# Kernel tuning notes

Hardware: AMD Instinct MI355X
Metric: run time of the kernel (lower is better)

Reference implementation:

```python
import jax, jax.numpy as jnp
import numpy as np

N = 50000   # nodes
E = 600000  # edges (before self loops)
D = 128     # in = hidden = out channels
EPS = 1e-5


def setup_inputs() -> dict:
    key = jax.random.key(0)
    ks = jax.random.split(key, 12)
    s = 1.0 / np.sqrt(D)
    inp = {
        "x": jax.random.normal(ks[0], (N, D), jnp.float32),
        "edge_index": jax.random.randint(ks[1], (2, E), 0, N, dtype=jnp.int64),
        "W1": jax.random.normal(ks[2], (D, D), jnp.float32) * s,
        "b1": jnp.zeros((D,), jnp.float32),
        "g1": jnp.ones((D,), jnp.float32),
        "be1": jnp.zeros((D,), jnp.float32),
        "W2": jax.random.normal(ks[3], (D, D), jnp.float32) * s,
        "b2": jnp.zeros((D,), jnp.float32),
        "g2": jnp.ones((D,), jnp.float32),
        "be2": jnp.zeros((D,), jnp.float32),
        "W3": jax.random.normal(ks[4], (D, D), jnp.float32) * s,
        "b3": jnp.zeros((D,), jnp.float32),
    }
    return inp


def _layer_norm(h, g, b):
    mu = jnp.mean(h, axis=-1, keepdims=True)
    var = jnp.mean(jnp.square(h - mu), axis=-1, keepdims=True)
    return (h - mu) * jax.lax.rsqrt(var + EPS) * g + b


def _gcn_layer(h, src, dst, ew, W, b, fill):
    # PyG gcn_norm: append internal self loops with weight `fill`
    loop = jnp.arange(N, dtype=src.dtype)
    s = jnp.concatenate([src, loop])
    d = jnp.concatenate([dst, loop])
    w = jnp.concatenate([ew, jnp.full((N,), fill, h.dtype)])
    deg = jax.ops.segment_sum(w, d, num_segments=N)
    dinv = jnp.where(deg > 0, jax.lax.rsqrt(deg), 0.0)
    norm = dinv[s] * w * dinv[d]  # [E_tot]
    hw = h @ W                    # [N, D]
    out = jax.ops.segment_sum(norm[:, None] * hw[s], d, num_segments=N)
    return out + b


def reference(x, edge_index, W1, b1, g1, be1, W2, b2, g2, be2, W3, b3):
    # outer add_self_loops with edge_weight = 1 (edge_attr is None path)
    loop = jnp.arange(N, dtype=edge_index.dtype)
    src = jnp.concatenate([edge_index[0], loop])
    dst = jnp.concatenate([edge_index[1], loop])
    ew = jnp.ones((E + N,), x.dtype)

    residual = x
    h = _gcn_layer(x, src, dst, ew, W1, b1, 2.0)   # improved=True
    h = jax.nn.relu(_layer_norm(h, g1, be1))
    h = _gcn_layer(h, src, dst, ew, W2, b2, 2.0)   # improved=True
    h = jax.nn.relu(_layer_norm(h, g2, be2))
    h = _gcn_layer(h, src, dst, ew, W3, b3, 1.0)   # improved=False
    return h + residual
```

## Files before the change

kernel.cpp:

```cpp
#include <hip/hip_runtime.h>
#include <hip/hip_bf16.h>
#include <cstdint>

#define N_NODES 50000
#define N_EDGES 600000
#define DCH     128
#define LN_EPS  1e-5f
#define CAP     64
#define CAPSH   6
#define SLICE_N (N_NODES + 1)

typedef __attribute__((ext_vector_type(8))) __bf16 bf16x8;
typedef __attribute__((ext_vector_type(4))) float  f32x4;
typedef __attribute__((ext_vector_type(4))) int          int4e;
typedef __attribute__((ext_vector_type(2))) unsigned int uint2e;

__device__ inline unsigned short f2bf(float f) {
    unsigned int b; __builtin_memcpy(&b, &f, 4);
    b = b + 0x7fffu + ((b >> 16) & 1u);
    return (unsigned short)(b >> 16);
}
__device__ inline float bf_lo(unsigned int u) {
    unsigned int t = u << 16; float f; __builtin_memcpy(&f, &t, 4); return f;
}
__device__ inline float bf_hi(unsigned int u) {
    unsigned int t = u & 0xffff0000u; float f; __builtin_memcpy(&f, &t, 4); return f;
}

__global__ __launch_bounds__(256) void fill_k(const int* __restrict__ ei,
                                              int* __restrict__ cnt, int* __restrict__ csr) {
    __shared__ int sbad;
    int tid = threadIdx.x;
    if (tid == 0) sbad = 0;
    __syncthreads();
    const long long* e64 = (const long long*)ei;
    long long v = e64[tid];
    long long w = e64[300000 + tid];
    if (v < 0 || v >= N_NODES || w < 0 || w >= N_NODES) sbad = 1;
    __syncthreads();
    int is64 = (sbad == 0);

    int e = blockIdx.x * 256 + tid;
    if (e >= N_EDGES) return;
    long long sv = is64 ? e64[e]           : (long long)ei[e];
    long long dv = is64 ? e64[N_EDGES + e] : (long long)ei[N_EDGES + e];
    int s = (int)(sv < 0 ? 0 : (sv >= N_NODES ? N_NODES - 1 : sv));
    int d = (int)(dv < 0 ? 0 : (dv >= N_NODES ? N_NODES - 1 : dv));
    int pos = atomicAdd(&cnt[d], 1);
    if (pos < CAP) csr[(d << CAPSH) + pos] = s;
}

#define CVT_T    ((N_NODES + 1) * 32)
#define DINV_OFF CVT_T
#define TRAN_OFF (DINV_OFF + N_NODES)
#define SENT_OFF (TRAN_OFF + 3 * 128 * 128)
#define PREP_T   (SENT_OFF + 128)

__global__ __launch_bounds__(256) void prep_k(
        const float* __restrict__ x, const int* __restrict__ cnt,
        const float* __restrict__ W1, const float* __restrict__ W2,
        const float* __restrict__ W3,
        unsigned short* __restrict__ xbf, float* __restrict__ dinv2,
        float* __restrict__ dinv1, unsigned short* __restrict__ Wt,
        unsigned short* __restrict__ hbuf) {
    int id = blockIdx.x * 256 + threadIdx.x;
    if (id < CVT_T) {
        int node = id >> 5;
        int co = (id & 31) * 4;
        int slice = co >> 5, off = co & 31;
        uint2 r; r.x = 0u; r.y = 0u;
        if (node < N_NODES) {
            float4 v = *(const float4*)(x + (size_t)node * DCH + co);
            float d = rsqrtf((float)cnt[node] + 3.0f);
            r.x = ((unsigned int)f2bf(v.y * d) << 16) | (unsigned int)f2bf(v.x * d);
            r.y = ((unsigned int)f2bf(v.w * d) << 16) | (unsigned int)f2bf(v.z * d);
        }
        *(uint2*)(xbf + ((size_t)slice * SLICE_N + node) * 32 + off) = r;
    } else if (id < TRAN_OFF) {
        int i = id - DINV_OFF;
        float c = (float)cnt[i];
        dinv2[i] = rsqrtf(c + 3.0f);
        dinv1[i] = rsqrtf(c + 2.0f);
    } else if (id < SENT_OFF) {
        int t = id - TRAN_OFF;
        int mat = t >> 14;
        int o = t & 16383;
        int n = o >> 7, k = o & 127;
        const float* W = (mat == 0) ? W1 : ((mat == 1) ? W2 : W3);
        Wt[t] = f2bf(W[k * 128 + n]);
    } else if (id < PREP_T) {
        int i = id - SENT_OFF;
        hbuf[((size_t)(i >> 5) * SLICE_N + N_NODES) * 32 + (i & 31)] = 0;
    }
}


__global__ __launch_bounds__(128) void agg_k(
        const unsigned short* __restrict__ hs, unsigned short* __restrict__ outb,
        const int* __restrict__ cnt, const int* __restrict__ csr,
        const float* __restrict__ dinv, float fillp1) {
    int slice = blockIdx.x & 3;
    int grp   = blockIdx.x >> 2;
    int wv    = threadIdx.x >> 6;
    int lane  = threadIdx.x & 63;
    int g     = lane >> 3;
    int l8    = lane & 7;
    int node  = grp * 16 + wv * 8 + g;

    const uint2* hp = (const uint2*)(hs + (size_t)slice * SLICE_N * 32);
    float di = dinv[node];
    int cn = cnt[node];
    int pc = (cn + 3) & ~3; if (pc > CAP) pc = CAP;
    pc = max(pc, __shfl_xor(pc, 8));
    pc = max(pc, __shfl_xor(pc, 16));
    pc = max(pc, __shfl_xor(pc, 32));

    const int4e* pcsr = (const int4e*)(csr + ((size_t)node << CAPSH));
    float a[4][4];
    #pragma unroll
    for (int j = 0; j < 4; j++)
        #pragma unroll
        for (int ch = 0; ch < 4; ch++) a[j][ch] = 0.f;

    for (int i = 0; i < pc; i += 4) {
        int4e e4 = __builtin_nontemporal_load(&pcsr[i >> 2]);
        int e0 = (i + 0 < cn) ? e4.x : N_NODES;
        int e1 = (i + 1 < cn) ? e4.y : N_NODES;
        int e2 = (i + 2 < cn) ? e4.z : N_NODES;
        int e3 = (i + 3 < cn) ? e4.w : N_NODES;
        uint2 u0 = hp[(size_t)e0 * 8 + l8];
        uint2 u1 = hp[(size_t)e1 * 8 + l8];
        uint2 u2 = hp[(size_t)e2 * 8 + l8];
        uint2 u3 = hp[(size_t)e3 * 8 + l8];
        a[0][0] += bf_lo(u0.x); a[0][1] += bf_hi(u0.x); a[0][2] += bf_lo(u0.y); a[0][3] += bf_hi(u0.y);
        a[1][0] += bf_lo(u1.x); a[1][1] += bf_hi(u1.x); a[1][2] += bf_lo(u1.y); a[1][3] += bf_hi(u1.y);
        a[2][0] += bf_lo(u2.x); a[2][1] += bf_hi(u2.x); a[2][2] += bf_lo(u2.y); a[2][3] += bf_hi(u2.y);
        a[3][0] += bf_lo(u3.x); a[3][1] += bf_hi(u3.x); a[3][2] += bf_lo(u3.y); a[3][3] += bf_hi(u3.y);
    }
    float c0 = (a[0][0] + a[1][0]) + (a[2][0] + a[3][0]);
    float c1 = (a[0][1] + a[1][1]) + (a[2][1] + a[3][1]);
    float c2 = (a[0][2] + a[1][2]) + (a[2][2] + a[3][2]);
    float c3 = (a[0][3] + a[1][3]) + (a[2][3] + a[3][3]);
    uint2 us = hp[(size_t)node * 8 + l8];
    c0 = di * (c0 + fillp1 * bf_lo(us.x));
    c1 = di * (c1 + fillp1 * bf_hi(us.x));
    c2 = di * (c2 + fillp1 * bf_lo(us.y));
    c3 = di * (c3 + fillp1 * bf_hi(us.y));
    uint2e res;
    res.x = ((unsigned int)f2bf(c1) << 16) | (unsigned int)f2bf(c0);
    res.y = ((unsigned int)f2bf(c3) << 16) | (unsigned int)f2bf(c2);
    __builtin_nontemporal_store(res,
        (uint2e*)(outb + (size_t)slice * SLICE_N * 32) + (size_t)node * 8 + l8);
}


template<int MODE>
__global__ __launch_bounds__(256) void gemm_k(
        const unsigned short* __restrict__ A,
        const unsigned short* __restrict__ Wt,
        const float* __restrict__ bias,
        const float* __restrict__ gamma,
        const float* __restrict__ beta,
        const float* __restrict__ dnext,
        const float* __restrict__ resid,
        unsigned short* __restrict__ out_bf,
        float* __restrict__ out_f) {
    int lane = threadIdx.x & 63;
    int wv   = threadIdx.x >> 6;
    int r0   = (blockIdx.x * 4 + wv) * 32;
    int m = lane & 15, q = lane >> 4;

    bf16x8 afr[2][4];
    #pragma unroll
    for (int mt = 0; mt < 2; mt++) {
        int arow = r0 + mt * 16 + m; if (arow >= N_NODES) arow = N_NODES - 1;
        #pragma unroll
        for (int kt = 0; kt < 4; kt++)
            afr[mt][kt] = __builtin_nontemporal_load(
                (const bf16x8*)(A + ((size_t)kt * SLICE_N + arow) * 32 + q * 8));
    }

    f32x4 acc[2][8];
    #pragma unroll
    for (int nt = 0; nt < 8; nt++) {
        f32x4 c0 = {0.f,0.f,0.f,0.f}, c1 = {0.f,0.f,0.f,0.f};
        const unsigned short* bp = Wt + (size_t)(nt * 16 + m) * DCH + q * 8;
        #pragma unroll
        for (int kt = 0; kt < 4; kt++) {
            bf16x8 bfr = *(const bf16x8*)(bp + kt * 32);
            c0 = __builtin_amdgcn_mfma_f32_16x16x32_bf16(afr[0][kt], bfr, c0, 0, 0, 0);
            c1 = __builtin_amdgcn_mfma_f32_16x16x32_bf16(afr[1][kt], bfr, c1, 0, 0, 0);
        }
        acc[0][nt] = c0; acc[1][nt] = c1;
    }

    float bv[8];
    #pragma unroll
    for (int nt = 0; nt < 8; nt++) bv[nt] = bias[nt * 16 + m];

    if (MODE == 0) {
        float gv[8], bev[8];
        #pragma unroll
        for (int nt = 0; nt < 8; nt++) { gv[nt] = gamma[nt*16+m]; bev[nt] = beta[nt*16+m]; }
        #pragma unroll
        for (int mt = 0; mt < 2; mt++) {
            #pragma unroll
            for (int nt = 0; nt < 8; nt++)
                #pragma unroll
                for (int r = 0; r < 4; r++) acc[mt][nt][r] += bv[nt];
            #pragma unroll
            for (int r = 0; r < 4; r++) {
                float s = 0.f, qs = 0.f;
                #pragma unroll
                for (int nt = 0; nt < 8; nt++) { float v = acc[mt][nt][r]; s += v; qs += v*v; }
                #pragma unroll
                for (int msk = 1; msk < 16; msk <<= 1) {
                    s  += __shfl_xor(s,  msk, 16);
                    qs += __shfl_xor(qs, msk, 16);
                }
                float mean = s * (1.f / 128.f);
                float var  = fmaxf(qs * (1.f / 128.f) - mean * mean, 0.f);
                float rstd = rsqrtf(var + LN_EPS);
                int row = r0 + mt * 16 + q * 4 + r;
                if (row < N_NODES) {
                    float dscale = dnext[row];
                    #pragma unroll
                    for (int nt = 0; nt < 8; nt++) {
                        float v = (acc[mt][nt][r] - mean) * rstd * gv[nt] + bev[nt];
                        v = fmaxf(v, 0.f) * dscale;
                        __builtin_nontemporal_store(f2bf(v),
                            out_bf + ((size_t)(nt >> 1) * SLICE_N + row) * 32
                                   + (nt & 1) * 16 + m);
                    }
                }
            }
        }
    } else {
        #pragma unroll
        for (int mt = 0; mt < 2; mt++)
            #pragma unroll
            for (int r = 0; r < 4; r++) {
                int row = r0 + mt * 16 + q * 4 + r;
                if (row < N_NODES) {
                    #pragma unroll
                    for (int nt = 0; nt < 8; nt++) {
                        float v = acc[mt][nt][r] + bv[nt]
                                + resid[(size_t)row * DCH + nt * 16 + m];
                        out_f[(size_t)row * DCH + nt * 16 + m] = v;
                    }
                }
            }
    }
}


extern "C" void kernel_launch(void* const* d_in, const int* in_sizes, int n_in,
                              void* d_out, int out_size, void* d_ws, size_t ws_size,
                              hipStream_t stream) {
    const float* x   = (const float*)d_in[0];
    const int*   ei  = (const int*)d_in[1];
    const float* W1  = (const float*)d_in[2];
    const float* b1  = (const float*)d_in[3];
    const float* g1  = (const float*)d_in[4];
    const float* be1 = (const float*)d_in[5];
    const float* W2  = (const float*)d_in[6];
    const float* b2  = (const float*)d_in[7];
    const float* g2  = (const float*)d_in[8];
    const float* be2 = (const float*)d_in[9];
    const float* W3  = (const float*)d_in[10];
    const float* b3  = (const float*)d_in[11];
    float* out = (float*)d_out;

    char* p = (char*)d_ws;
    auto alloc = [&](size_t bytes) -> void* {
        void* r = (void*)p; p += (bytes + 255) & ~(size_t)255; return r;
    };
    int*   cnt   = (int*)  alloc((size_t)N_NODES * 4);
    float* dinv2 = (float*)alloc((size_t)N_NODES * 4);
    float* dinv1 = (float*)alloc((size_t)N_NODES * 4);
    int*   csr   = (int*)  alloc((size_t)N_NODES * CAP * 4);
    unsigned short* Wt   = (unsigned short*)alloc((size_t)3 * 128 * 128 * 2);
    unsigned short* aggb = (unsigned short*)alloc((size_t)4 * SLICE_N * 32 * 2);
    unsigned short* xbf  = (unsigned short*)alloc((size_t)4 * SLICE_N * 32 * 2);
    unsigned short* hbuf = (unsigned short*)alloc((size_t)4 * SLICE_N * 32 * 2);

    (void)hipMemsetAsync(cnt, 0, (size_t)N_NODES * 4, stream);
    fill_k<<<(N_EDGES + 255) / 256, 256, 0, stream>>>(ei, cnt, csr);
    prep_k<<<(PREP_T + 255) / 256, 256, 0, stream>>>(x, cnt, W1, W2, W3,
                                                     xbf, dinv2, dinv1, Wt, hbuf);

    const int A_BLOCKS = 3125 * 4;
    const int G_BLOCKS = (N_NODES + 127) / 128;

    agg_k<<<A_BLOCKS, 128, 0, stream>>>(xbf, aggb, cnt, csr, dinv2, 3.0f);
    gemm_k<0><<<G_BLOCKS, 256, 0, stream>>>(aggb, Wt, b1, g1, be1, dinv2, nullptr, hbuf, nullptr);
    agg_k<<<A_BLOCKS, 128, 0, stream>>>(hbuf, aggb, cnt, csr, dinv2, 3.0f);
    gemm_k<0><<<G_BLOCKS, 256, 0, stream>>>(aggb, Wt + 16384, b2, g2, be2, dinv1, nullptr, hbuf, nullptr);
    agg_k<<<A_BLOCKS, 128, 0, stream>>>(hbuf, aggb, cnt, csr, dinv1, 2.0f);
    gemm_k<1><<<G_BLOCKS, 256, 0, stream>>>(aggb, Wt + 32768, b3, nullptr, nullptr, nullptr, x, nullptr, out);
}
```

Before: 298.0 us.

## Split CSR into four 16-slot buckets with uint16 indices, shrink GEMM row tile

```diff
diff --git a/kernel.cpp b/kernel.cpp
--- a/kernel.cpp
+++ b/kernel.cpp
@@ -8,11 +8,12 @@
 #define LN_EPS  1e-5f
 #define CAP     64
 #define CAPSH   6
+#define BCAP    16
 #define SLICE_N (N_NODES + 1)
 
 typedef __attribute__((ext_vector_type(8))) __bf16 bf16x8;
 typedef __attribute__((ext_vector_type(4))) float  f32x4;
-typedef __attribute__((ext_vector_type(4))) int          int4e;
+typedef __attribute__((ext_vector_type(8))) unsigned short u16x8;
 typedef __attribute__((ext_vector_type(2))) unsigned int uint2e;
 
 __device__ inline unsigned short f2bf(float f) {
@@ -28,7 +29,8 @@
 }
 
 __global__ __launch_bounds__(256) void fill_k(const int* __restrict__ ei,
-                                              int* __restrict__ cnt, int* __restrict__ csr) {
+                                              int* __restrict__ cnt4,
+                                              unsigned short* __restrict__ csr) {
     __shared__ int sbad;
     int tid = threadIdx.x;
     if (tid == 0) sbad = 0;
@@ -46,8 +48,9 @@
     long long dv = is64 ? e64[N_EDGES + e] : (long long)ei[N_EDGES + e];
     int s = (int)(sv < 0 ? 0 : (sv >= N_NODES ? N_NODES - 1 : sv));
     int d = (int)(dv < 0 ? 0 : (dv >= N_NODES ? N_NODES - 1 : dv));
-    int pos = atomicAdd(&cnt[d], 1);
-    if (pos < CAP) csr[(d << CAPSH) + pos] = s;
+    int b = e & 3;
+    int pos = atomicAdd(&cnt4[b * N_NODES + d], 1);
+    if (pos < BCAP) csr[(d << CAPSH) + (b << 4) + pos] = (unsigned short)s;
 }
 
 #define CVT_T    ((N_NODES + 1) * 32)
@@ -57,7 +60,7 @@
 #define PREP_T   (SENT_OFF + 128)
 
 __global__ __launch_bounds__(256) void prep_k(
-        const float* __restrict__ x, const int* __restrict__ cnt,
+        const float* __restrict__ x, const int* __restrict__ cnt4,
         const float* __restrict__ W1, const float* __restrict__ W2,
         const float* __restrict__ W3,
         unsigned short* __restrict__ xbf, float* __restrict__ dinv2,
@@ -71,16 +74,19 @@
         uint2 r; r.x = 0u; r.y = 0u;
         if (node < N_NODES) {
             float4 v = *(const float4*)(x + (size_t)node * DCH + co);
-            float d = rsqrtf((float)cnt[node] + 3.0f);
+            int c = cnt4[node] + cnt4[N_NODES + node]
+                  + cnt4[2 * N_NODES + node] + cnt4[3 * N_NODES + node];
+            float d = rsqrtf((float)c + 3.0f);
             r.x = ((unsigned int)f2bf(v.y * d) << 16) | (unsigned int)f2bf(v.x * d);
             r.y = ((unsigned int)f2bf(v.w * d) << 16) | (unsigned int)f2bf(v.z * d);
         }
         *(uint2*)(xbf + ((size_t)slice * SLICE_N + node) * 32 + off) = r;
     } else if (id < TRAN_OFF) {
         int i = id - DINV_OFF;
-        float c = (float)cnt[i];
-        dinv2[i] = rsqrtf(c + 3.0f);
-        dinv1[i] = rsqrtf(c + 2.0f);
+        int c = cnt4[i] + cnt4[N_NODES + i]
+              + cnt4[2 * N_NODES + i] + cnt4[3 * N_NODES + i];
+        dinv2[i] = rsqrtf((float)c + 3.0f);
+        dinv1[i] = rsqrtf((float)c + 2.0f);
     } else if (id < SENT_OFF) {
         int t = id - TRAN_OFF;
         int mat = t >> 14;
@@ -94,10 +100,9 @@
     }
 }
 
-
 __global__ __launch_bounds__(128) void agg_k(
         const unsigned short* __restrict__ hs, unsigned short* __restrict__ outb,
-        const int* __restrict__ cnt, const int* __restrict__ csr,
+        const int* __restrict__ cnt4, const unsigned short* __restrict__ csr,
         const float* __restrict__ dinv, float fillp1) {
     int slice = blockIdx.x & 3;
     int grp   = blockIdx.x >> 2;
@@ -109,46 +114,74 @@
 
     const uint2* hp = (const uint2*)(hs + (size_t)slice * SLICE_N * 32);
     float di = dinv[node];
-    int cn = cnt[node];
-    int pc = (cn + 3) & ~3; if (pc > CAP) pc = CAP;
-    pc = max(pc, __shfl_xor(pc, 8));
-    pc = max(pc, __shfl_xor(pc, 16));
-    pc = max(pc, __shfl_xor(pc, 32));
-
-    const int4e* pcsr = (const int4e*)(csr + ((size_t)node << CAPSH));
+    int bc0 = min(cnt4[node], BCAP);
+    int bc1 = min(cnt4[N_NODES + node], BCAP);
+    int bc2 = min(cnt4[2 * N_NODES + node], BCAP);
+    int bc3 = min(cnt4[3 * N_NODES + node], BCAP);
+
+    const u16x8* pcsr = (const u16x8*)(csr + ((size_t)node << CAPSH));
+    u16x8 c0 = __builtin_nontemporal_load(pcsr + 0);
+    u16x8 c1 = __builtin_nontemporal_load(pcsr + 2);
+    u16x8 c2 = __builtin_nontemporal_load(pcsr + 4);
+    u16x8 c3 = __builtin_nontemporal_load(pcsr + 6);
+
     float a[4][4];
     #pragma unroll
-    for (int j = 0; j < 4; j++)
-        #pragma unroll
-        for (int ch = 0; ch < 4; ch++) a[j][ch] = 0.f;
-
-    for (int i = 0; i < pc; i += 4) {
-        int4e e4 = __builtin_nontemporal_load(&pcsr[i >> 2]);
-        int e0 = (i + 0 < cn) ? e4.x : N_NODES;
-        int e1 = (i + 1 < cn) ? e4.y : N_NODES;
-        int e2 = (i + 2 < cn) ? e4.z : N_NODES;
-        int e3 = (i + 3 < cn) ? e4.w : N_NODES;
-        uint2 u0 = hp[(size_t)e0 * 8 + l8];
-        uint2 u1 = hp[(size_t)e1 * 8 + l8];
-        uint2 u2 = hp[(size_t)e2 * 8 + l8];
-        uint2 u3 = hp[(size_t)e3 * 8 + l8];
-        a[0][0] += bf_lo(u0.x); a[0][1] += bf_hi(u0.x); a[0][2] += bf_lo(u0.y); a[0][3] += bf_hi(u0.y);
-        a[1][0] += bf_lo(u1.x); a[1][1] += bf_hi(u1.x); a[1][2] += bf_lo(u1.y); a[1][3] += bf_hi(u1.y);
-        a[2][0] += bf_lo(u2.x); a[2][1] += bf_hi(u2.x); a[2][2] += bf_lo(u2.y); a[2][3] += bf_hi(u2.y);
-        a[3][0] += bf_lo(u3.x); a[3][1] += bf_hi(u3.x); a[3][2] += bf_lo(u3.y); a[3][3] += bf_hi(u3.y);
-    }
-    float c0 = (a[0][0] + a[1][0]) + (a[2][0] + a[3][0]);
-    float c1 = (a[0][1] + a[1][1]) + (a[2][1] + a[3][1]);
-    float c2 = (a[0][2] + a[1][2]) + (a[2][2] + a[3][2]);
-    float c3 = (a[0][3] + a[1][3]) + (a[2][3] + a[3][3]);
+    for (int k = 0; k < 4; k++)
+        #pragma unroll
+        for (int ch = 0; ch < 4; ch++) a[k][ch] = 0.f;
+
+    int eidx[32];
+    #pragma unroll
+    for (int j = 0; j < 8; j++) {
+        eidx[j]      = (j < bc0) ? (int)c0[j] : N_NODES;
+        eidx[8 + j]  = (j < bc1) ? (int)c1[j] : N_NODES;
+        eidx[16 + j] = (j < bc2) ? (int)c2[j] : N_NODES;
+        eidx[24 + j] = (j < bc3) ? (int)c3[j] : N_NODES;
+    }
+    #pragma unroll
+    for (int t = 0; t < 32; t++) {
+        uint2 u = hp[(size_t)eidx[t] * 8 + l8];
+        int k = t & 3;
+        a[k][0] += bf_lo(u.x); a[k][1] += bf_hi(u.x);
+        a[k][2] += bf_lo(u.y); a[k][3] += bf_hi(u.y);
+    }
+
+    int bm = max(max(bc0, bc1), max(bc2, bc3));
+    if (__any(bm > 8)) {
+        u16x8 d0 = __builtin_nontemporal_load(pcsr + 1);
+        u16x8 d1 = __builtin_nontemporal_load(pcsr + 3);
+        u16x8 d2 = __builtin_nontemporal_load(pcsr + 5);
+        u16x8 d3 = __builtin_nontemporal_load(pcsr + 7);
+        int fidx[32];
+        #pragma unroll
+        for (int j = 0; j < 8; j++) {
+            fidx[j]      = (8 + j < bc0) ? (int)d0[j] : N_NODES;
+            fidx[8 + j]  = (8 + j < bc1) ? (int)d1[j] : N_NODES;
+            fidx[16 + j] = (8 + j < bc2) ? (int)d2[j] : N_NODES;
+            fidx[24 + j] = (8 + j < bc3) ? (int)d3[j] : N_NODES;
+        }
+        #pragma unroll
+        for (int t = 0; t < 32; t++) {
+            uint2 u = hp[(size_t)fidx[t] * 8 + l8];
+            int k = t & 3;
+            a[k][0] += bf_lo(u.x); a[k][1] += bf_hi(u.x);
+            a[k][2] += bf_lo(u.y); a[k][3] += bf_hi(u.y);
+        }
+    }
+
+    float s0 = (a[0][0] + a[1][0]) + (a[2][0] + a[3][0]);
+    float s1 = (a[0][1] + a[1][1]) + (a[2][1] + a[3][1]);
+    float s2 = (a[0][2] + a[1][2]) + (a[2][2] + a[3][2]);
+    float s3 = (a[0][3] + a[1][3]) + (a[2][3] + a[3][3]);
     uint2 us = hp[(size_t)node * 8 + l8];
-    c0 = di * (c0 + fillp1 * bf_lo(us.x));
-    c1 = di * (c1 + fillp1 * bf_hi(us.x));
-    c2 = di * (c2 + fillp1 * bf_lo(us.y));
-    c3 = di * (c3 + fillp1 * bf_hi(us.y));
+    s0 = di * (s0 + fillp1 * bf_lo(us.x));
+    s1 = di * (s1 + fillp1 * bf_hi(us.x));
+    s2 = di * (s2 + fillp1 * bf_lo(us.y));
+    s3 = di * (s3 + fillp1 * bf_hi(us.y));
     uint2e res;
-    res.x = ((unsigned int)f2bf(c1) << 16) | (unsigned int)f2bf(c0);
-    res.y = ((unsigned int)f2bf(c3) << 16) | (unsigned int)f2bf(c2);
+    res.x = ((unsigned int)f2bf(s1) << 16) | (unsigned int)f2bf(s0);
+    res.y = ((unsigned int)f2bf(s3) << 16) | (unsigned int)f2bf(s2);
     __builtin_nontemporal_store(res,
         (uint2e*)(outb + (size_t)slice * SLICE_N * 32) + (size_t)node * 8 + l8);
 }
@@ -167,31 +200,27 @@
         float* __restrict__ out_f) {
     int lane = threadIdx.x & 63;
     int wv   = threadIdx.x >> 6;
-    int r0   = (blockIdx.x * 4 + wv) * 32;
+    int r0   = (blockIdx.x * 4 + wv) * 16;
     int m = lane & 15, q = lane >> 4;
 
-    bf16x8 afr[2][4];
-    #pragma unroll
-    for (int mt = 0; mt < 2; mt++) {
-        int arow = r0 + mt * 16 + m; if (arow >= N_NODES) arow = N_NODES - 1;
-        #pragma unroll
-        for (int kt = 0; kt < 4; kt++)
-            afr[mt][kt] = __builtin_nontemporal_load(
-                (const bf16x8*)(A + ((size_t)kt * SLICE_N + arow) * 32 + q * 8));
-    }
-
-    f32x4 acc[2][8];
+    bf16x8 afr[4];
+    int arow = r0 + m; if (arow >= N_NODES) arow = N_NODES - 1;
+    #pragma unroll
+    for (int kt = 0; kt < 4; kt++)
+        afr[kt] = __builtin_nontemporal_load(
+            (const bf16x8*)(A + ((size_t)kt * SLICE_N + arow) * 32 + q * 8));
+
+    f32x4 acc[8];
     #pragma unroll
     for (int nt = 0; nt < 8; nt++) {
-        f32x4 c0 = {0.f,0.f,0.f,0.f}, c1 = {0.f,0.f,0.f,0.f};
+        f32x4 c0 = {0.f, 0.f, 0.f, 0.f};
         const unsigned short* bp = Wt + (size_t)(nt * 16 + m) * DCH + q * 8;
         #pragma unroll
         for (int kt = 0; kt < 4; kt++) {
             bf16x8 bfr = *(const bf16x8*)(bp + kt * 32);
-            c0 = __builtin_amdgcn_mfma_f32_16x16x32_bf16(afr[0][kt], bfr, c0, 0, 0, 0);
-            c1 = __builtin_amdgcn_mfma_f32_16x16x32_bf16(afr[1][kt], bfr, c1, 0, 0, 0);
-        }
-        acc[0][nt] = c0; acc[1][nt] = c1;
+            c0 = __builtin_amdgcn_mfma_f32_16x16x32_bf16(afr[kt], bfr, c0, 0, 0, 0);
+        }
+        acc[nt] = c0;
     }
 
     float bv[8];
@@ -203,53 +232,48 @@
         #pragma unroll
         for (int nt = 0; nt < 8; nt++) { gv[nt] = gamma[nt*16+m]; bev[nt] = beta[nt*16+m]; }
         #pragma unroll
-        for (int mt = 0; mt < 2; mt++) {
+        for (int nt = 0; nt < 8; nt++)
             #pragma unroll
-            for (int nt = 0; nt < 8; nt++)
+            for (int r = 0; r < 4; r++) acc[nt][r] += bv[nt];
+        #pragma unroll
+        for (int r = 0; r < 4; r++) {
+            float s = 0.f, qs = 0.f;
+            #pragma unroll
+            for (int nt = 0; nt < 8; nt++) { float v = acc[nt][r]; s += v; qs += v*v; }
+            #pragma unroll
+            for (int msk = 1; msk < 16; msk <<= 1) {
+                s  += __shfl_xor(s,  msk, 16);
+                qs += __shfl_xor(qs, msk, 16);
+            }
+            float mean = s * (1.f / 128.f);
+            float var  = fmaxf(qs * (1.f / 128.f) - mean * mean, 0.f);
+            float rstd = rsqrtf(var + LN_EPS);
+            int row = r0 + q * 4 + r;
+            if (row < N_NODES) {
+                float dscale = dnext[row];
                 #pragma unroll
-                for (int r = 0; r < 4; r++) acc[mt][nt][r] += bv[nt];
-            #pragma unroll
-            for (int r = 0; r < 4; r++) {
-                float s = 0.f, qs = 0.f;
-                #pragma unroll
-                for (int nt = 0; nt < 8; nt++) { float v = acc[mt][nt][r]; s += v; qs += v*v; }
-                #pragma unroll
-                for (int msk = 1; msk < 16; msk <<= 1) {
-                    s  += __shfl_xor(s,  msk, 16);
-                    qs += __shfl_xor(qs, msk, 16);
-                }
-                float mean = s * (1.f / 128.f);
-                float var  = fmaxf(qs * (1.f / 128.f) - mean * mean, 0.f);
-                float rstd = rsqrtf(var + LN_EPS);
-                int row = r0 + mt * 16 + q * 4 + r;
-                if (row < N_NODES) {
-                    float dscale = dnext[row];
-                    #pragma unroll
-                    for (int nt = 0; nt < 8; nt++) {
-                        float v = (acc[mt][nt][r] - mean) * rstd * gv[nt] + bev[nt];
-                        v = fmaxf(v, 0.f) * dscale;
-                        __builtin_nontemporal_store(f2bf(v),
-                            out_bf + ((size_t)(nt >> 1) * SLICE_N + row) * 32
-                                   + (nt & 1) * 16 + m);
-                    }
+                for (int nt = 0; nt < 8; nt++) {
+                    float v = (acc[nt][r] - mean) * rstd * gv[nt] + bev[nt];
+                    v = fmaxf(v, 0.f) * dscale;
+                    __builtin_nontemporal_store(f2bf(v),
+                        out_bf + ((size_t)(nt >> 1) * SLICE_N + row) * 32
+                               + (nt & 1) * 16 + m);
                 }
             }
         }
     } else {
         #pragma unroll
-        for (int mt = 0; mt < 2; mt++)
-            #pragma unroll
-            for (int r = 0; r < 4; r++) {
-                int row = r0 + mt * 16 + q * 4 + r;
-                if (row < N_NODES) {
-                    #pragma unroll
-                    for (int nt = 0; nt < 8; nt++) {
-                        float v = acc[mt][nt][r] + bv[nt]
-                                + resid[(size_t)row * DCH + nt * 16 + m];
-                        out_f[(size_t)row * DCH + nt * 16 + m] = v;
-                    }
+        for (int r = 0; r < 4; r++) {
+            int row = r0 + q * 4 + r;
+            if (row < N_NODES) {
+                #pragma unroll
+                for (int nt = 0; nt < 8; nt++) {
+                    float v = acc[nt][r] + bv[nt]
+                            + resid[(size_t)row * DCH + nt * 16 + m];
+                    out_f[(size_t)row * DCH + nt * 16 + m] = v;
                 }
             }
+        }
     }
 }
 
@@ -275,27 +299,27 @@
     auto alloc = [&](size_t bytes) -> void* {
         void* r = (void*)p; p += (bytes + 255) & ~(size_t)255; return r;
     };
-    int*   cnt   = (int*)  alloc((size_t)N_NODES * 4);
+    int*   cnt4  = (int*)  alloc((size_t)4 * N_NODES * 4);
     float* dinv2 = (float*)alloc((size_t)N_NODES * 4);
     float* dinv1 = (float*)alloc((size_t)N_NODES * 4);
-    int*   csr   = (int*)  alloc((size_t)N_NODES * CAP * 4);
+    unsigned short* csr = (unsigned short*)alloc((size_t)N_NODES * CAP * 2);
     unsigned short* Wt   = (unsigned short*)alloc((size_t)3 * 128 * 128 * 2);
     unsigned short* aggb = (unsigned short*)alloc((size_t)4 * SLICE_N * 32 * 2);
     unsigned short* xbf  = (unsigned short*)alloc((size_t)4 * SLICE_N * 32 * 2);
     unsigned short* hbuf = (unsigned short*)alloc((size_t)4 * SLICE_N * 32 * 2);
 
-    (void)hipMemsetAsync(cnt, 0, (size_t)N_NODES * 4, stream);
-    fill_k<<<(N_EDGES + 255) / 256, 256, 0, stream>>>(ei, cnt, csr);
-    prep_k<<<(PREP_T + 255) / 256, 256, 0, stream>>>(x, cnt, W1, W2, W3,
+    (void)hipMemsetAsync(cnt4, 0, (size_t)4 * N_NODES * 4, stream);
+    fill_k<<<(N_EDGES + 255) / 256, 256, 0, stream>>>(ei, cnt4, csr);
+    prep_k<<<(PREP_T + 255) / 256, 256, 0, stream>>>(x, cnt4, W1, W2, W3,
                                                      xbf, dinv2, dinv1, Wt, hbuf);
 
     const int A_BLOCKS = 3125 * 4;
-    const int G_BLOCKS = (N_NODES + 127) / 128;
-
-    agg_k<<<A_BLOCKS, 128, 0, stream>>>(xbf, aggb, cnt, csr, dinv2, 3.0f);
+    const int G_BLOCKS = (N_NODES + 63) / 64;
+
+    agg_k<<<A_BLOCKS, 128, 0, stream>>>(xbf, aggb, cnt4, csr, dinv2, 3.0f);
     gemm_k<0><<<G_BLOCKS, 256, 0, stream>>>(aggb, Wt, b1, g1, be1, dinv2, nullptr, hbuf, nullptr);
-    agg_k<<<A_BLOCKS, 128, 0, stream>>>(hbuf, aggb, cnt, csr, dinv2, 3.0f);
+    agg_k<<<A_BLOCKS, 128, 0, stream>>>(hbuf, aggb, cnt4, csr, dinv2, 3.0f);
     gemm_k<0><<<G_BLOCKS, 256, 0, stream>>>(aggb, Wt + 16384, b2, g2, be2, dinv1, nullptr, hbuf, nullptr);
-    agg_k<<<A_BLOCKS, 128, 0, stream>>>(hbuf, aggb, cnt, csr, dinv1, 2.0f);
+    agg_k<<<A_BLOCKS, 128, 0, stream>>>(hbuf, aggb, cnt4, csr, dinv1, 2.0f);
     gemm_k<1><<<G_BLOCKS, 256, 0, stream>>>(aggb, Wt + 32768, b3, nullptr, nullptr, nullptr, x, nullptr, out);
 }
```

New measurement: 325.7 us. 1.09x slower.
